# Kernel tuning notes

Measured on AMD Instinct MI355X. Metric: run time of the kernel, lower is better.

Reference implementation:

```python
import jax, jax.numpy as jnp
import numpy as np

BOUND = 1.0
DENSITY_SCALE = 1.0
MIN_NEAR = 0.2
EPS = 1e-15


def setup_inputs() -> dict:
    key = jax.random.key(0)
    ks = jax.random.split(key, 10)
    N, H = 32768, 32
    rays_o = (jax.random.uniform(ks[0], (N, 3), jnp.float32) - 0.5)  # inside AABB
    rays_d = jax.random.normal(ks[1], (N, 3), jnp.float32)
    W1 = jax.random.normal(ks[2], (3, H), jnp.float32) * 0.5
    b1 = jnp.zeros((H,), jnp.float32)
    Wsig = jax.random.normal(ks[3], (H, 1), jnp.float32) * 0.5
    Wsig_d = jax.random.normal(ks[4], (H, 1), jnp.float32) * 0.5
    Wc1 = jax.random.normal(ks[5], (6, H), jnp.float32) * 0.5
    bc1 = jnp.zeros((H,), jnp.float32)
    Wc2 = jax.random.normal(ks[6], (H, 3), jnp.float32) * 0.5
    Wc2_d = jax.random.normal(ks[7], (H, 3), jnp.float32) * 0.5
    return {"rays_o": rays_o, "rays_d": rays_d, "W1": W1, "b1": b1,
            "Wsig": Wsig, "Wsig_d": Wsig_d, "Wc1": Wc1, "bc1": bc1,
            "Wc2": Wc2, "Wc2_d": Wc2_d, "num_steps": 128}


def _composite(deltas, sigma, z01, rgbs):
    # alphas / transmittance / weights, as in run()
    alphas = 1.0 - jnp.exp(-deltas * DENSITY_SCALE * sigma)           # [N,T]
    shifted = jnp.concatenate([jnp.ones_like(alphas[..., :1]),
                               1.0 - alphas + EPS], axis=-1)
    weights = alphas * jnp.cumprod(shifted, axis=-1)[..., :-1]        # [N,T]
    ws = weights.sum(axis=-1)                                          # [N]
    depth = jnp.sum(weights * z01, axis=-1)                            # [N]
    image = jnp.sum(weights[..., None] * rgbs, axis=-2)                # [N,3]
    image = image + (1.0 - ws)[..., None] * 1.0  # bg_color = 1
    return image, depth, ws


def reference(rays_o, rays_d, W1, b1, Wsig, Wsig_d, Wc1, bc1, Wc2, Wc2_d, num_steps):
    N = rays_o.shape[0]
    T = num_steps
    d = rays_d / jnp.linalg.norm(rays_d, axis=-1, keepdims=True)
    # near_far_from_aabb (slab test), aabb = [-1,1]^3
    inv = 1.0 / d
    t1 = (-BOUND - rays_o) * inv
    t2 = (BOUND - rays_o) * inv
    near = jnp.max(jnp.minimum(t1, t2), axis=-1, keepdims=True)        # [N,1]
    far = jnp.min(jnp.maximum(t1, t2), axis=-1, keepdims=True)
    near = jnp.maximum(near, MIN_NEAR)
    far = jnp.maximum(far, near + 1e-6)
    z = jnp.linspace(0.0, 1.0, T, dtype=rays_o.dtype)[None, :]
    z_vals = near + (far - near) * z                                    # [N,T]
    sample_dist = (far - near) / T                                      # [N,1]
    xyzs = rays_o[:, None, :] + d[:, None, :] * z_vals[..., None]       # [N,T,3]
    xyzs = jnp.clip(xyzs, -BOUND, BOUND)
    # surrogate density MLP (shared trunk, main + dummy heads)
    h = jax.nn.relu(jnp.einsum('ntc,ch->nth', xyzs, W1) + b1)           # [N,T,H]
    sigma = jax.nn.softplus(jnp.einsum('nth,ho->nt', h, Wsig))          # [N,T]
    sigma_dummy = jax.nn.softplus(jnp.einsum('nth,ho->nt', h, Wsig_d))
    # deltas
    deltas = z_vals[..., 1:] - z_vals[..., :-1]
    deltas = jnp.concatenate([deltas, sample_dist * jnp.ones_like(deltas[..., :1])], axis=-1)
    # surrogate color MLP on (xyz, dir)
    dirs = jnp.broadcast_to(d[:, None, :], xyzs.shape)
    feat = jnp.concatenate([xyzs, dirs], axis=-1)                       # [N,T,6]
    hc = jax.nn.relu(jnp.einsum('ntc,ch->nth', feat, Wc1) + bc1)
    rgbs = jax.nn.sigmoid(jnp.einsum('nth,hc->ntc', hc, Wc2))           # [N,T,3]
    rgbs_dummy = jax.nn.sigmoid(jnp.einsum('nth,hc->ntc', hc, Wc2_d))
    z01 = jnp.clip((z_vals - near) / (far - near), 0.0, 1.0)
    image, depth, ws = _composite(deltas, sigma, z01, rgbs)
    image_d, depth_d, _ = _composite(deltas, sigma_dummy, z01, rgbs_dummy)
    # pack: image(3) | depth(1) | weights_sum(1) | image_dummy(3) | depth_dummy(1)
    return jnp.concatenate([image, depth[:, None], ws[:, None],
                            image_d, depth_d[:, None]], axis=-1)        # [N,9]
```

## Files before the change

kernel.cpp:

```cpp
#include <hip/hip_runtime.h>
#include <hip/hip_bf16.h>


typedef float  f32x4  __attribute__((ext_vector_type(4)));
typedef short  bf16x8 __attribute__((ext_vector_type(8)));
typedef unsigned int u32;

__device__ __forceinline__ float fast_rcp(float x){ return __builtin_amdgcn_rcpf(x); }
__device__ __forceinline__ float softplus_f(float x){
    float e = __expf(-fabsf(x));
    return fmaxf(x,0.f) + __logf(1.f+e);
}
__device__ __forceinline__ float sigmoid_f(float x){ return fast_rcp(1.f+__expf(-x)); }

__device__ __forceinline__ u32 pktr(float lo, float hi){
    return __builtin_amdgcn_perm(__float_as_uint(hi), __float_as_uint(lo), 0x07060302u);
}
__device__ __forceinline__ u32 bfr_hi(float f){
    u32 u = __float_as_uint(f);
    return (u + 0x7FFFu + ((u>>16)&1u)) & 0xFFFF0000u;
}
__device__ __forceinline__ u32 pkbf(float lo, float hi){
    return (bfr_hi(lo)>>16) | bfr_hi(hi);
}

__global__ __launch_bounds__(256)
void nerf_prep_kernel(const float* __restrict__ W1, const float* __restrict__ b1,
                      const float* __restrict__ Wsig, const float* __restrict__ Wsig_d,
                      const float* __restrict__ Wc1, const float* __restrict__ bc1,
                      const float* __restrict__ Wc2, const float* __restrict__ Wc2_d,
                      u32* __restrict__ ws)
{
    const int q0 = threadIdx.x;
#pragma unroll
    for (int k = 0; k < 6; ++k) {
        const int q = q0 + k*256;
        u32 val = 0u;
        if (q < 1024) {
            const int ut = q>>8, rem = q&255, lane = rem>>2, dw = rem&3;
            const int g = lane>>4, m = lane&15;
            if (g == 0) {
                float w[8];
                if (ut < 2) { const int u = ut*16 + m;
                    w[0]=W1[u];  w[1]=W1[32+u];  w[2]=W1[64+u];  w[3]=b1[u];
                    w[4]=0.f;    w[5]=0.f;       w[6]=0.f;       w[7]=0.f;
                } else {        const int u = (ut-2)*16 + m;
                    w[0]=Wc1[u]; w[1]=Wc1[32+u]; w[2]=Wc1[64+u]; w[3]=bc1[u];
                    w[4]=Wc1[96+u]; w[5]=Wc1[128+u]; w[6]=Wc1[160+u]; w[7]=0.f;
                }
                val = pkbf(w[2*dw], w[2*dw+1]);
            }
        } else {
            const int q2 = q-1024, ch = q2>>8, rem = q2&255, lane = rem>>2, dw = rem&3;
            const int g = lane>>4, o = lane&15;
            float w[2];
#pragma unroll
            for (int e = 0; e < 2; ++e) {
                const int kk = 2*dw + e;
                const int h = kk>>2, rr = kk&3;
                const int u_local = h*16 + g*4 + rr;
                float v = 0.f;
                if (ch == 0) {
                    if (o == 0) v = Wsig[u_local];
                    else if (o == 1) v = Wsig_d[u_local];
                } else {
                    if (o >= 2 && o <= 4) v = Wc2[u_local*3 + (o-2)];
                    else if (o >= 5 && o <= 7) v = Wc2_d[u_local*3 + (o-5)];
                }
                w[e] = v;
            }
            val = pkbf(w[0], w[1]);
        }
        ws[q] = val;
    }
}

#define PSTR 4
#define SSTR 12
#define WSTR 1024
#define CSTR 100
#define LOG2E 1.44269504088896340736f

__global__ __launch_bounds__(512, 6)
void nerf_render_kernel(const float* __restrict__ rays_o,
                        const float* __restrict__ rays_d,
                        const u32*  __restrict__ wsm,
                        const int*  __restrict__ num_steps,
                        float* __restrict__ out,
                        int N)
{
    __shared__ u32 smem[8 * WSTR];

    const int tid  = threadIdx.x;
    const int seg  = tid>>6, lane = tid&63;
    const int ray  = blockIdx.x*64 + lane;
    const int rayc = (ray < N) ? ray : (N-1);
    const int T = num_steps[0];
    const int g = lane>>4, c = lane&15;

    u32*   posW   = smem + seg*WSTR;
    float* stashW = (float*)(smem + seg*WSTR + 64*PSTR);
    float* comb   = (float*)smem;

    const uint4* wsv = (const uint4*)wsm;
    uint4 a1u0 = wsv[0*64 + lane];
    uint4 a1u1 = wsv[1*64 + lane];
    uint4 a1u2 = wsv[2*64 + lane];
    uint4 a1u3 = wsv[3*64 + lane];
    uint4 a2u0 = wsv[256 + 0*64 + lane];
    uint4 a2u1 = wsv[256 + 1*64 + lane];
    asm volatile("" : "+v"(a1u0.x), "+v"(a1u0.y), "+v"(a1u0.z), "+v"(a1u0.w),
                      "+v"(a1u1.x), "+v"(a1u1.y), "+v"(a1u1.z), "+v"(a1u1.w),
                      "+v"(a1u2.x), "+v"(a1u2.y), "+v"(a1u2.z), "+v"(a1u2.w));
    asm volatile("" : "+v"(a1u3.x), "+v"(a1u3.y), "+v"(a1u3.z), "+v"(a1u3.w),
                      "+v"(a2u0.x), "+v"(a2u0.y), "+v"(a2u0.z), "+v"(a2u0.w),
                      "+v"(a2u1.x), "+v"(a2u1.y), "+v"(a2u1.z), "+v"(a2u1.w));

    const float ox = rays_o[rayc*3+0], oy = rays_o[rayc*3+1], oz = rays_o[rayc*3+2];
    const float rdx = rays_d[rayc*3+0], rdy = rays_d[rayc*3+1], rdz = rays_d[rayc*3+2];
    const float rn = rsqrtf(rdx*rdx + rdy*rdy + rdz*rdz);
    const float dx = rdx*rn, dy = rdy*rn, dz = rdz*rn;

    const float ix = 1.0f/dx, iy = 1.0f/dy, iz = 1.0f/dz;
    const float t1x = (-1.f-ox)*ix, t2x = (1.f-ox)*ix;
    const float t1y = (-1.f-oy)*iy, t2y = (1.f-oy)*iy;
    const float t1z = (-1.f-oz)*iz, t2z = (1.f-oz)*iz;
    float nearv = fmaxf(fmaxf(fminf(t1x,t2x), fminf(t1y,t2y)), fminf(t1z,t2z));
    float farv  = fminf(fminf(fmaxf(t1x,t2x), fmaxf(t1y,t2y)), fmaxf(t1z,t2z));
    nearv = fmaxf(nearv, 0.2f);
    farv  = fmaxf(farv, nearv + 1e-6f);

    const float span    = farv - nearv;
    const float stepz   = (T > 1) ? span/(float)(T-1) : 0.f;
    const float inv_tm1 = (T > 1) ? 1.f/(float)(T-1) : 0.f;
    const float last_dt = span/(float)T;
    const float nStep2  = -stepz  * LOG2E;
    const float nLast2  = -last_dt * LOG2E;

    const u32 dirw0 = pkbf(dx, dy);
    const u32 dirw1 = pkbf(dz, 0.f);

    const int Sper = (T + 7) >> 3;
    const int segStart = seg * Sper;
    const int segEnd = (segStart + Sper < T) ? (segStart + Sper) : T;
    const int nch = (segEnd > segStart) ? (segEnd - segStart) : 0;

    const int posOff = 4*c;
    const int stOff  = c*SSTR + g*4;

    float iA0=0.f,iA1=0.f,iA2=0.f,dAc=0.f,wsA=0.f,TAx=1.f;
    float iD0=0.f,iD1=0.f,iD2=0.f,dDc=0.f,wsD=0.f,TDx=1.f;
    const f32x4 z4 = {0.f,0.f,0.f,0.f};

    for (int cs = 0; cs < nch; ++cs) {
        const int tg = segStart + cs;

        {
            const float zv = fmaf(stepz, (float)tg, nearv);
            const float X = fminf(fmaxf(fmaf(dx, zv, ox), -1.f), 1.f);
            const float Y = fminf(fmaxf(fmaf(dy, zv, oy), -1.f), 1.f);
            const float Z = fminf(fmaxf(fmaf(dz, zv, oz), -1.f), 1.f);
            uint4 v;
            v.x = pktr(X, Y);
            v.y = pktr(Z, 1.0f);
            v.z = dirw0;
            v.w = dirw1;
            *(uint4*)&posW[lane*PSTR] = v;
        }

        __builtin_amdgcn_s_setprio(1);
#define TILEB(TAU)                                                                \
        {                                                                         \
            const uint4 b1u = *(const uint4*)&posW[(TAU)*(16*PSTR) + posOff];     \
            const bf16x8 b1f = __builtin_bit_cast(bf16x8, b1u);                   \
            f32x4 acc10 = __builtin_amdgcn_mfma_f32_16x16x32_bf16(                \
                __builtin_bit_cast(bf16x8, a1u0), b1f, z4, 0,0,0);                \
            f32x4 acc11 = __builtin_amdgcn_mfma_f32_16x16x32_bf16(                \
                __builtin_bit_cast(bf16x8, a1u1), b1f, z4, 0,0,0);                \
            f32x4 acc12 = __builtin_amdgcn_mfma_f32_16x16x32_bf16(                \
                __builtin_bit_cast(bf16x8, a1u2), b1f, z4, 0,0,0);                \
            f32x4 acc13 = __builtin_amdgcn_mfma_f32_16x16x32_bf16(                \
                __builtin_bit_cast(bf16x8, a1u3), b1f, z4, 0,0,0);                \
            const f32x4 r0 = __builtin_elementwise_max(acc10, z4);                \
            const f32x4 r1 = __builtin_elementwise_max(acc11, z4);                \
            const f32x4 r2 = __builtin_elementwise_max(acc12, z4);                \
            const f32x4 r3 = __builtin_elementwise_max(acc13, z4);                \
            uint4 b2a, b2b;                                                       \
            b2a.x = pktr(r0.x, r0.y);  b2a.y = pktr(r0.z, r0.w);                  \
            b2a.z = pktr(r1.x, r1.y);  b2a.w = pktr(r1.z, r1.w);                  \
            b2b.x = pktr(r2.x, r2.y);  b2b.y = pktr(r2.z, r2.w);                  \
            b2b.z = pktr(r3.x, r3.y);  b2b.w = pktr(r3.z, r3.w);                  \
            f32x4 acc2 = __builtin_amdgcn_mfma_f32_16x16x32_bf16(                 \
                __builtin_bit_cast(bf16x8, a2u0), __builtin_bit_cast(bf16x8, b2a),\
                z4, 0, 0, 0);                                                     \
            acc2 = __builtin_amdgcn_mfma_f32_16x16x32_bf16(                       \
                __builtin_bit_cast(bf16x8, a2u1), __builtin_bit_cast(bf16x8, b2b),\
                acc2, 0, 0, 0);                                                   \
            if (g < 2) {                                                          \
                *(f32x4*)&stashW[(TAU)*(16*SSTR) + stOff] = acc2;                 \
            }                                                                     \
        }
        TILEB(0) TILEB(1) TILEB(2) TILEB(3)
#undef TILEB
        __builtin_amdgcn_s_setprio(0);

        {
            const f32x4 oA = *(const f32x4*)&stashW[lane*SSTR];
            const f32x4 oB = *(const f32x4*)&stashW[lane*SSTR + 4];
            const float dneg2 = (tg < T-1) ? nStep2 : nLast2;
            const float z01   = (float)tg * inv_tm1;

            const float sigA = softplus_f(oA.x);
            const float qA = exp2f(dneg2*sigA);
            const float wA = TAx - TAx*qA; TAx *= qA;
            iA0 = fmaf(wA, sigmoid_f(oA.z), iA0);
            iA1 = fmaf(wA, sigmoid_f(oA.w), iA1);
            iA2 = fmaf(wA, sigmoid_f(oB.x), iA2);
            dAc = fmaf(wA, z01, dAc); wsA += wA;

            const float sigD = softplus_f(oA.y);
            const float qD = exp2f(dneg2*sigD);
            const float wD = TDx - TDx*qD; TDx *= qD;
            iD0 = fmaf(wD, sigmoid_f(oB.y), iD0);
            iD1 = fmaf(wD, sigmoid_f(oB.z), iD1);
            iD2 = fmaf(wD, sigmoid_f(oB.w), iD2);
            dDc = fmaf(wD, z01, dDc); wsD += wD;
        }
    }

    __syncthreads();
    *(f32x4*)&comb[lane*CSTR + seg*12 + 0] = (f32x4){iA0, iA1, iA2, dAc};
    *(f32x4*)&comb[lane*CSTR + seg*12 + 4] = (f32x4){wsA, TAx, iD0, iD1};
    *(f32x4*)&comb[lane*CSTR + seg*12 + 8] = (f32x4){iD2, dDc, wsD, TDx};
    __syncthreads();

    if (seg == 0 && ray < N) {
        float tA = TAx, tD = TDx;
#pragma unroll
        for (int s = 1; s < 8; ++s) {
            const f32x4 v0 = *(const f32x4*)&comb[lane*CSTR + s*12 + 0];
            const f32x4 v1 = *(const f32x4*)&comb[lane*CSTR + s*12 + 4];
            const f32x4 v2 = *(const f32x4*)&comb[lane*CSTR + s*12 + 8];
            iA0 = fmaf(tA, v0.x, iA0);
            iA1 = fmaf(tA, v0.y, iA1);
            iA2 = fmaf(tA, v0.z, iA2);
            dAc = fmaf(tA, v0.w, dAc);
            wsA = fmaf(tA, v1.x, wsA);
            tA *= v1.y;
            iD0 = fmaf(tD, v1.z, iD0);
            iD1 = fmaf(tD, v1.w, iD1);
            iD2 = fmaf(tD, v2.x, iD2);
            dDc = fmaf(tD, v2.y, dDc);
            wsD = fmaf(tD, v2.z, wsD);
            tD *= v2.w;
        }
        const float bgA = 1.f - wsA;
        const float bgD = 1.f - wsD;
        float* o = out + (size_t)ray * 9;
        o[0] = iA0 + bgA;
        o[1] = iA1 + bgA;
        o[2] = iA2 + bgA;
        o[3] = dAc;
        o[4] = wsA;
        o[5] = iD0 + bgD;
        o[6] = iD1 + bgD;
        o[7] = iD2 + bgD;
        o[8] = dDc;
    }
}

extern "C" void kernel_launch(void* const* d_in, const int* in_sizes, int n_in,
                              void* d_out, int out_size, void* d_ws, size_t ws_size,
                              hipStream_t stream) {
    const float* rays_o = (const float*)d_in[0];
    const float* rays_d = (const float*)d_in[1];
    const float* W1     = (const float*)d_in[2];
    const float* b1     = (const float*)d_in[3];
    const float* Wsig   = (const float*)d_in[4];
    const float* Wsig_d = (const float*)d_in[5];
    const float* Wc1    = (const float*)d_in[6];
    const float* bc1    = (const float*)d_in[7];
    const float* Wc2    = (const float*)d_in[8];
    const float* Wc2_d  = (const float*)d_in[9];
    const int* num_steps = (const int*)d_in[10];

    const int N = in_sizes[0] / 3;
    float* out = (float*)d_out;
    u32*   ws  = (u32*)d_ws;

    hipLaunchKernelGGL(nerf_prep_kernel, dim3(1), dim3(256), 0, stream,
                       W1, b1, Wsig, Wsig_d, Wc1, bc1, Wc2, Wc2_d, ws);

    const int blocks = (N + 63) / 64;
    hipLaunchKernelGGL(nerf_render_kernel, dim3(blocks), dim3(512), 0, stream,
                       rays_o, rays_d, ws, num_steps, out, N);
}
```

Before: 52.18 us.

## Process two sample steps per iteration with double-buffered LDS slots

Unrolls the per-wave sample loop by two. Each step gets its own position and stash slot in shared memory, so the position writes, MFMA tiles and compositing of two steps can be interleaved for more instruction-level parallelism. The per-wave LDS region doubles to 64 KB per block and the launch-bounds occupancy hint drops from 6 to 4. This may reduce occupancy and adds a tail branch for an odd step count.

```diff
diff --git a/kernel.cpp b/kernel.cpp
--- a/kernel.cpp
+++ b/kernel.cpp
@@ -77,11 +77,12 @@
 
 #define PSTR 4
 #define SSTR 12
-#define WSTR 1024
+#define SLOT 1024
+#define WSTR 2048
 #define CSTR 100
 #define LOG2E 1.44269504088896340736f
 
-__global__ __launch_bounds__(512, 6)
+__global__ __launch_bounds__(512, 4)
 void nerf_render_kernel(const float* __restrict__ rays_o,
                         const float* __restrict__ rays_d,
                         const u32*  __restrict__ wsm,
@@ -98,9 +99,11 @@
     const int T = num_steps[0];
     const int g = lane>>4, c = lane&15;
 
-    u32*   posW   = smem + seg*WSTR;
-    float* stashW = (float*)(smem + seg*WSTR + 64*PSTR);
-    float* comb   = (float*)smem;
+    u32*   posW0   = smem + seg*WSTR;
+    float* stash0  = (float*)(posW0 + 64*PSTR);
+    u32*   posW1   = posW0 + SLOT;
+    float* stash1  = (float*)(posW1 + 64*PSTR);
+    float* comb    = (float*)smem;
 
     const uint4* wsv = (const uint4*)wsm;
     uint4 a1u0 = wsv[0*64 + lane];
@@ -152,81 +155,97 @@
     float iD0=0.f,iD1=0.f,iD2=0.f,dDc=0.f,wsD=0.f,TDx=1.f;
     const f32x4 z4 = {0.f,0.f,0.f,0.f};
 
-    for (int cs = 0; cs < nch; ++cs) {
-        const int tg = segStart + cs;
-
-        {
-            const float zv = fmaf(stepz, (float)tg, nearv);
-            const float X = fminf(fmaxf(fmaf(dx, zv, ox), -1.f), 1.f);
-            const float Y = fminf(fmaxf(fmaf(dy, zv, oy), -1.f), 1.f);
-            const float Z = fminf(fmaxf(fmaf(dz, zv, oz), -1.f), 1.f);
-            uint4 v;
-            v.x = pktr(X, Y);
-            v.y = pktr(Z, 1.0f);
-            v.z = dirw0;
-            v.w = dirw1;
-            *(uint4*)&posW[lane*PSTR] = v;
+#define PHASEA(TG, PW)                                                            \
+    {                                                                             \
+        const float zv = fmaf(stepz, (float)(TG), nearv);                         \
+        const float X = fminf(fmaxf(fmaf(dx, zv, ox), -1.f), 1.f);                \
+        const float Y = fminf(fmaxf(fmaf(dy, zv, oy), -1.f), 1.f);                \
+        const float Z = fminf(fmaxf(fmaf(dz, zv, oz), -1.f), 1.f);                \
+        uint4 v;                                                                  \
+        v.x = pktr(X, Y);                                                         \
+        v.y = pktr(Z, 1.0f);                                                      \
+        v.z = dirw0;                                                              \
+        v.w = dirw1;                                                              \
+        *(uint4*)&(PW)[lane*PSTR] = v;                                            \
+    }
+
+#define TILEB(TAU, PW, SW)                                                        \
+    {                                                                             \
+        const uint4 b1u = *(const uint4*)&(PW)[(TAU)*(16*PSTR) + posOff];         \
+        const bf16x8 b1f = __builtin_bit_cast(bf16x8, b1u);                       \
+        f32x4 acc10 = __builtin_amdgcn_mfma_f32_16x16x32_bf16(                    \
+            __builtin_bit_cast(bf16x8, a1u0), b1f, z4, 0,0,0);                    \
+        f32x4 acc11 = __builtin_amdgcn_mfma_f32_16x16x32_bf16(                    \
+            __builtin_bit_cast(bf16x8, a1u1), b1f, z4, 0,0,0);                    \
+        f32x4 acc12 = __builtin_amdgcn_mfma_f32_16x16x32_bf16(                    \
+            __builtin_bit_cast(bf16x8, a1u2), b1f, z4, 0,0,0);                    \
+        f32x4 acc13 = __builtin_amdgcn_mfma_f32_16x16x32_bf16(                    \
+            __builtin_bit_cast(bf16x8, a1u3), b1f, z4, 0,0,0);                    \
+        const f32x4 r0 = __builtin_elementwise_max(acc10, z4);                    \
+        const f32x4 r1 = __builtin_elementwise_max(acc11, z4);                    \
+        const f32x4 r2 = __builtin_elementwise_max(acc12, z4);                    \
+        const f32x4 r3 = __builtin_elementwise_max(acc13, z4);                    \
+        uint4 b2a, b2b;                                                           \
+        b2a.x = pktr(r0.x, r0.y);  b2a.y = pktr(r0.z, r0.w);                      \
+        b2a.z = pktr(r1.x, r1.y);  b2a.w = pktr(r1.z, r1.w);                      \
+        b2b.x = pktr(r2.x, r2.y);  b2b.y = pktr(r2.z, r2.w);                      \
+        b2b.z = pktr(r3.x, r3.y);  b2b.w = pktr(r3.z, r3.w);                      \
+        f32x4 acc2 = __builtin_amdgcn_mfma_f32_16x16x32_bf16(                     \
+            __builtin_bit_cast(bf16x8, a2u0), __builtin_bit_cast(bf16x8, b2a),    \
+            z4, 0, 0, 0);                                                         \
+        acc2 = __builtin_amdgcn_mfma_f32_16x16x32_bf16(                           \
+            __builtin_bit_cast(bf16x8, a2u1), __builtin_bit_cast(bf16x8, b2b),    \
+            acc2, 0, 0, 0);                                                       \
+        if (g < 2) {                                                              \
+            *(f32x4*)&(SW)[(TAU)*(16*SSTR) + stOff] = acc2;                       \
+        }                                                                         \
+    }
+
+#define PHASEC(TG, SW)                                                            \
+    {                                                                             \
+        const f32x4 oA = *(const f32x4*)&(SW)[lane*SSTR];                         \
+        const f32x4 oB = *(const f32x4*)&(SW)[lane*SSTR + 4];                     \
+        const float dneg2 = ((TG) < T-1) ? nStep2 : nLast2;                       \
+        const float z01   = (float)(TG) * inv_tm1;                                \
+        const float sigA = softplus_f(oA.x);                                      \
+        const float qA = exp2f(dneg2*sigA);                                       \
+        const float wA = TAx - TAx*qA; TAx *= qA;                                 \
+        iA0 = fmaf(wA, sigmoid_f(oA.z), iA0);                                     \
+        iA1 = fmaf(wA, sigmoid_f(oA.w), iA1);                                     \
+        iA2 = fmaf(wA, sigmoid_f(oB.x), iA2);                                     \
+        dAc = fmaf(wA, z01, dAc); wsA += wA;                                      \
+        const float sigD = softplus_f(oA.y);                                      \
+        const float qD = exp2f(dneg2*sigD);                                       \
+        const float wD = TDx - TDx*qD; TDx *= qD;                                 \
+        iD0 = fmaf(wD, sigmoid_f(oB.y), iD0);                                     \
+        iD1 = fmaf(wD, sigmoid_f(oB.z), iD1);                                     \
+        iD2 = fmaf(wD, sigmoid_f(oB.w), iD2);                                     \
+        dDc = fmaf(wD, z01, dDc); wsD += wD;                                      \
+    }
+
+    for (int cs = 0; cs < nch; cs += 2) {
+        const int tg0 = segStart + cs;
+        const int tg1 = tg0 + 1;
+        const bool has2 = (cs + 1 < nch);
+
+        PHASEA(tg0, posW0)
+        if (has2) PHASEA(tg1, posW1)
+
+        __builtin_amdgcn_s_setprio(1);
+        TILEB(0, posW0, stash0) TILEB(1, posW0, stash0)
+        TILEB(2, posW0, stash0) TILEB(3, posW0, stash0)
+        if (has2) {
+            TILEB(0, posW1, stash1) TILEB(1, posW1, stash1)
+            TILEB(2, posW1, stash1) TILEB(3, posW1, stash1)
         }
-
-        __builtin_amdgcn_s_setprio(1);
-#define TILEB(TAU)                                                                \
-        {                                                                         \
-            const uint4 b1u = *(const uint4*)&posW[(TAU)*(16*PSTR) + posOff];     \
-            const bf16x8 b1f = __builtin_bit_cast(bf16x8, b1u);                   \
-            f32x4 acc10 = __builtin_amdgcn_mfma_f32_16x16x32_bf16(                \
-                __builtin_bit_cast(bf16x8, a1u0), b1f, z4, 0,0,0);                \
-            f32x4 acc11 = __builtin_amdgcn_mfma_f32_16x16x32_bf16(                \
-                __builtin_bit_cast(bf16x8, a1u1), b1f, z4, 0,0,0);                \
-            f32x4 acc12 = __builtin_amdgcn_mfma_f32_16x16x32_bf16(                \
-                __builtin_bit_cast(bf16x8, a1u2), b1f, z4, 0,0,0);                \
-            f32x4 acc13 = __builtin_amdgcn_mfma_f32_16x16x32_bf16(                \
-                __builtin_bit_cast(bf16x8, a1u3), b1f, z4, 0,0,0);                \
-            const f32x4 r0 = __builtin_elementwise_max(acc10, z4);                \
-            const f32x4 r1 = __builtin_elementwise_max(acc11, z4);                \
-            const f32x4 r2 = __builtin_elementwise_max(acc12, z4);                \
-            const f32x4 r3 = __builtin_elementwise_max(acc13, z4);                \
-            uint4 b2a, b2b;                                                       \
-            b2a.x = pktr(r0.x, r0.y);  b2a.y = pktr(r0.z, r0.w);                  \
-            b2a.z = pktr(r1.x, r1.y);  b2a.w = pktr(r1.z, r1.w);                  \
-            b2b.x = pktr(r2.x, r2.y);  b2b.y = pktr(r2.z, r2.w);                  \
-            b2b.z = pktr(r3.x, r3.y);  b2b.w = pktr(r3.z, r3.w);                  \
-            f32x4 acc2 = __builtin_amdgcn_mfma_f32_16x16x32_bf16(                 \
-                __builtin_bit_cast(bf16x8, a2u0), __builtin_bit_cast(bf16x8, b2a),\
-                z4, 0, 0, 0);                                                     \
-            acc2 = __builtin_amdgcn_mfma_f32_16x16x32_bf16(                       \
-                __builtin_bit_cast(bf16x8, a2u1), __builtin_bit_cast(bf16x8, b2b),\
-                acc2, 0, 0, 0);                                                   \
-            if (g < 2) {                                                          \
-                *(f32x4*)&stashW[(TAU)*(16*SSTR) + stOff] = acc2;                 \
-            }                                                                     \
-        }
-        TILEB(0) TILEB(1) TILEB(2) TILEB(3)
+        __builtin_amdgcn_s_setprio(0);
+
+        PHASEC(tg0, stash0)
+        if (has2) PHASEC(tg1, stash1)
+    }
+#undef PHASEA
 #undef TILEB
-        __builtin_amdgcn_s_setprio(0);
-
-        {
-            const f32x4 oA = *(const f32x4*)&stashW[lane*SSTR];
-            const f32x4 oB = *(const f32x4*)&stashW[lane*SSTR + 4];
-            const float dneg2 = (tg < T-1) ? nStep2 : nLast2;
-            const float z01   = (float)tg * inv_tm1;
-
-            const float sigA = softplus_f(oA.x);
-            const float qA = exp2f(dneg2*sigA);
-            const float wA = TAx - TAx*qA; TAx *= qA;
-            iA0 = fmaf(wA, sigmoid_f(oA.z), iA0);
-            iA1 = fmaf(wA, sigmoid_f(oA.w), iA1);
-            iA2 = fmaf(wA, sigmoid_f(oB.x), iA2);
-            dAc = fmaf(wA, z01, dAc); wsA += wA;
-
-            const float sigD = softplus_f(oA.y);
-            const float qD = exp2f(dneg2*sigD);
-            const float wD = TDx - TDx*qD; TDx *= qD;
-            iD0 = fmaf(wD, sigmoid_f(oB.y), iD0);
-            iD1 = fmaf(wD, sigmoid_f(oB.z), iD1);
-            iD2 = fmaf(wD, sigmoid_f(oB.w), iD2);
-            dDc = fmaf(wD, z01, dDc); wsD += wD;
-        }
-    }
+#undef PHASEC
 
     __syncthreads();
     *(f32x4*)&comb[lane*CSTR + seg*12 + 0] = (f32x4){iA0, iA1, iA2, dAc};
```

Measured after the change: 50.36 us (median of 2 runs). 3.5% less time.
